# Performance work log

Measured on AMD Instinct MI355X. Metric: run time of the kernel, lower is better.

Reference implementation:

```python
import jax, jax.numpy as jnp
import numpy as np

E4M3_MAX = 448.0  # fp8_max_fwd for Format.HYBRID fprop tensors
MARGIN = 0        # DelayedScaling default


def _quantize_e4m3(t, s):
    # cast_to_fp8: scale, saturate-cast to E4M3; amax of the unscaled tensor
    q = (t * s).astype(jnp.float8_e4m3fn)
    amax = jnp.max(jnp.abs(t))
    return q, amax


def _sf_compute(amax, scale, fp8_max, margin):
    # faithful port of _default_sf_compute (including its tf.where ordering)
    exp = jnp.floor(jnp.log2(fp8_max / amax)) - margin
    sf = jnp.round(jnp.exp2(jnp.abs(exp)))
    sf = jnp.where(amax > 0.0, sf, scale)
    sf = jnp.where(jnp.isinf(amax), sf, scale)
    sf = jnp.where(exp < 0, 1.0 / sf, sf)
    return sf


def setup_inputs() -> dict:
    key = jax.random.key(0)
    k1, k2 = jax.random.split(key)
    M, K, N = 16384, 2048, 2048
    x = jax.random.normal(k1, (M, K), dtype=jnp.float32)
    kernel = jax.random.normal(k2, (K, N), dtype=jnp.float32) * 0.02
    scale = jnp.ones((2,), dtype=jnp.float32)
    scale_inv = jnp.ones((2,), dtype=jnp.float32)
    amax_history = jnp.zeros((1, 2), dtype=jnp.float32)
    return {"x": x, "kernel": kernel, "scale": scale,
            "scale_inv": scale_inv, "amax_history": amax_history}


def reference(x, kernel, scale, scale_inv, amax_history):
    # --- cast_to_fp8 for activation (index 0) and weight (index 1) ---
    x_q, amax_x = _quantize_e4m3(x, scale[0])          # [M, K] fp8
    w_q, amax_w = _quantize_e4m3(kernel.T, scale[1])   # [N, K] fp8 (B in row-major, gemm does B^T)
    new_scale_inv = jnp.stack([1.0 / scale[0], 1.0 / scale[1]])
    # record amaxes into most-recent slot of the history
    amax_history = amax_history.at[0, 0].set(amax_x).at[0, 1].set(amax_w)

    # --- fp8_matmul: D = (A * A_scale_inv) @ (B * B_scale_inv)^T ---
    out = jnp.matmul(x_q.astype(jnp.float32), w_q.astype(jnp.float32).T)
    out = out * (new_scale_inv[0] * new_scale_inv[1])  # [M, N]

    # --- fused_amax_and_scale_update (amax_compute_algo='most_recent') ---
    amax = amax_history[0]
    rolled = jnp.roll(amax_history, -1, axis=0).at[0].set(0.0)
    new_scale = _sf_compute(amax, scale, E4M3_MAX, MARGIN)
    return out, new_scale, rolled
```

## Files before the change

kernel.cpp:

```cpp
#include <hip/hip_runtime.h>
#include <cstdint>

#define M_DIM 16384
#define K_DIM 2048
#define N_DIM 2048

typedef float f32x4 __attribute__((ext_vector_type(4)));
typedef int   i32x8 __attribute__((ext_vector_type(8)));

__global__ __launch_bounds__(256) void quant_x_kernel(
    const float4* __restrict__ x, uint4* __restrict__ xq,
    const float* __restrict__ scale, unsigned int* __restrict__ amax)
{
    const int gid = blockIdx.x * 256 + threadIdx.x;
    const float s = scale[0];
    float m = 0.0f;
#pragma unroll
    for (int j = 0; j < 8; ++j) {
        float4 v = x[gid + j * 1048576];
        m = fmaxf(m, fmaxf(fmaxf(fabsf(v.x), fabsf(v.y)),
                           fmaxf(fabsf(v.z), fabsf(v.w))));
        unsigned int p0 = __builtin_amdgcn_cvt_pk_fp8_f32(v.x * s, v.y * s, 0, false);
        unsigned int p  = __builtin_amdgcn_cvt_pk_fp8_f32(v.z * s, v.w * s, p0, true);
        ((unsigned int*)xq)[gid + j * 1048576] = p;
    }

#pragma unroll
    for (int off = 32; off > 0; off >>= 1)
        m = fmaxf(m, __shfl_down(m, off, 64));
    __shared__ float red[4];
    if ((threadIdx.x & 63) == 0) red[threadIdx.x >> 6] = m;
    __syncthreads();
    if (threadIdx.x == 0) {
        m = fmaxf(fmaxf(red[0], red[1]), fmaxf(red[2], red[3]));
        atomicMax(amax, __float_as_uint(m));
    }
}

__global__ __launch_bounds__(256) void quant_w_kernel(
    const float* __restrict__ w, uint8_t* __restrict__ wq,
    const float* __restrict__ scale, unsigned int* __restrict__ amax)
{
    __shared__ float tile[64][68];
    const int t = threadIdx.x;
    const int nb = blockIdx.x * 64;
    const int kb = blockIdx.y * 64;
    const float s = scale[1];
    float m = 0.0f;
#pragma unroll
    for (int j = 0; j < 4; ++j) {
        int f = j * 256 + t;
        int row = f >> 4;
        int c4 = f & 15;
        float4 v = *(const float4*)(w + (size_t)(kb + row) * N_DIM + nb + c4 * 4);
        m = fmaxf(m, fmaxf(fmaxf(fabsf(v.x), fabsf(v.y)),
                           fmaxf(fabsf(v.z), fabsf(v.w))));
        *(float4*)(&tile[row][c4 * 4]) = v;
    }
    __syncthreads();
    const int n = t >> 2, c = t & 3;
    unsigned int pk[4];
#pragma unroll
    for (int jj = 0; jj < 4; ++jj) {
        float f0 = tile[c * 16 + jj * 4 + 0][n] * s;
        float f1 = tile[c * 16 + jj * 4 + 1][n] * s;
        float f2 = tile[c * 16 + jj * 4 + 2][n] * s;
        float f3 = tile[c * 16 + jj * 4 + 3][n] * s;
        unsigned int p = __builtin_amdgcn_cvt_pk_fp8_f32(f0, f1, 0, false);
        pk[jj] = __builtin_amdgcn_cvt_pk_fp8_f32(f2, f3, p, true);
    }
    *(uint4*)(wq + (size_t)(nb + n) * K_DIM + kb + c * 16) = make_uint4(pk[0], pk[1], pk[2], pk[3]);

#pragma unroll
    for (int off = 32; off > 0; off >>= 1)
        m = fmaxf(m, __shfl_down(m, off, 64));
    __shared__ float red[4];
    if ((t & 63) == 0) red[t >> 6] = m;
    __syncthreads();
    if (t == 0) {
        m = fmaxf(fmaxf(red[0], red[1]), fmaxf(red[2], red[3]));
        atomicMax(amax, __float_as_uint(m));
    }
}

__global__ __launch_bounds__(256) void gemm_fp8_kernel(
    const uint8_t* __restrict__ Aq, const uint8_t* __restrict__ Bq,
    const float* __restrict__ scale, float* __restrict__ C)
{
    __shared__ uint8_t lds[65536];
    const int tid  = threadIdx.x;
    const int wave = tid >> 6;
    const int lane = tid & 63;
    const int wm = wave >> 1, wn = wave & 1;
    const int q = lane >> 4, r = lane & 15;

    const int blk = blockIdx.x;
    const int xcd = blk & 7;
    const int idx = blk >> 3;
    const int bm  = xcd * 16 + (idx >> 4);
    const int bn  = idx & 15;

    const size_t a_base = (size_t)bm * 128 * K_DIM;
    const size_t b_base = (size_t)bn * 128 * K_DIM;

    int srow[4], skoff[4], sdst[4];
#pragma unroll
    for (int j = 0; j < 4; ++j) {
        const int s = j * 4 + wave;
        srow[j]  = (s >> 1) * 16 + (lane & 15);
        skoff[j] = (lane >> 4) * 32 + (s & 1) * 16;
        sdst[j]  = s * 1024 + lane * 16;
    }

    f32x4 acc[4][4];
#pragma unroll
    for (int i = 0; i < 4; ++i)
#pragma unroll
        for (int j = 0; j < 4; ++j) acc[i][j] = (f32x4){0.f, 0.f, 0.f, 0.f};

    const int SONE = 0x7F7F7F7F;

    auto issue = [&](int kt, int b) {
        const size_t kg = (size_t)kt * 128;
        uint8_t* base = lds + b * 32768;
#pragma unroll
        for (int j = 0; j < 4; ++j) {
            const uint8_t* ga = Aq + a_base + (size_t)srow[j] * K_DIM + kg + skoff[j];
            const uint8_t* gb = Bq + b_base + (size_t)srow[j] * K_DIM + kg + skoff[j];
            __builtin_amdgcn_global_load_lds(
                (const __attribute__((address_space(1))) uint32_t*)ga,
                (__attribute__((address_space(3))) uint32_t*)(base + sdst[j]), 16, 0, 0);
            __builtin_amdgcn_global_load_lds(
                (const __attribute__((address_space(1))) uint32_t*)gb,
                (__attribute__((address_space(3))) uint32_t*)(base + 16384 + sdst[j]), 16, 0, 0);
        }
    };

    issue(0, 0);

    for (int kt = 0; kt < K_DIM / 128; ++kt) {
        __syncthreads();
        if (kt + 1 < K_DIM / 128) issue(kt + 1, (kt + 1) & 1);

        const uint8_t* base = lds + (kt & 1) * 32768;
        i32x8 a_frag[4], b_frag[4];
#pragma unroll
        for (int mi = 0; mi < 4; ++mi) {
            const uint8_t* pa = base + (wm * 4 + mi) * 2048 + lane * 16;
            int4 lo = *(const int4*)pa;
            int4 hi = *(const int4*)(pa + 1024);
            a_frag[mi] = (i32x8){lo.x, lo.y, lo.z, lo.w, hi.x, hi.y, hi.z, hi.w};
        }
#pragma unroll
        for (int ni = 0; ni < 4; ++ni) {
            const uint8_t* pb = base + 16384 + (wn * 4 + ni) * 2048 + lane * 16;
            int4 lo = *(const int4*)pb;
            int4 hi = *(const int4*)(pb + 1024);
            b_frag[ni] = (i32x8){lo.x, lo.y, lo.z, lo.w, hi.x, hi.y, hi.z, hi.w};
        }
#pragma unroll
        for (int mi = 0; mi < 4; ++mi)
#pragma unroll
            for (int ni = 0; ni < 4; ++ni)
                acc[mi][ni] = __builtin_amdgcn_mfma_scale_f32_16x16x128_f8f6f4(
                    a_frag[mi], b_frag[ni], acc[mi][ni],
                    0 , 0 ,
                    0, SONE, 0, SONE);
    }

    const float sinv = (1.0f / scale[0]) * (1.0f / scale[1]);
#pragma unroll
    for (int mi = 0; mi < 4; ++mi) {
#pragma unroll
        for (int ni = 0; ni < 4; ++ni) {
            const int col  = bn * 128 + wn * 64 + ni * 16 + r;
            const int row0 = bm * 128 + wm * 64 + mi * 16 + q * 4;
#pragma unroll
            for (int rr = 0; rr < 4; ++rr)
                __builtin_nontemporal_store(acc[mi][ni][rr] * sinv,
                    &C[(size_t)(row0 + rr) * N_DIM + col]);
        }
    }
}

__global__ void finalize_kernel(const float* __restrict__ scale,
                                const unsigned int* __restrict__ amax_bits,
                                float* __restrict__ out_tail)
{
    const int i = threadIdx.x;
    if (i < 2) {
        const float amax = __uint_as_float(amax_bits[i]);
        const float sc = scale[i];
        const float e = floorf(log2f(448.0f / amax));
        float sf = roundf(exp2f(fabsf(e)));
        sf = (amax > 0.0f) ? sf : sc;
        sf = isinf(amax) ? sf : sc;
        if (e < 0.0f) sf = 1.0f / sf;
        out_tail[i] = sf;
        out_tail[2 + i] = 0.0f;
    }
}

extern "C" void kernel_launch(void* const* d_in, const int* in_sizes, int n_in,
                              void* d_out, int out_size, void* d_ws, size_t ws_size,
                              hipStream_t stream)
{
    const float* x     = (const float*)d_in[0];
    const float* w     = (const float*)d_in[1];
    const float* scale = (const float*)d_in[2];

    uint8_t* ws = (uint8_t*)d_ws;
    uint8_t* xq = ws;
    uint8_t* wq = ws + (size_t)M_DIM * K_DIM;
    unsigned int* amax = (unsigned int*)(ws + (size_t)M_DIM * K_DIM + (size_t)N_DIM * K_DIM);

    hipMemsetAsync(amax, 0, 2 * sizeof(unsigned int), stream);

    quant_x_kernel<<<4096, 256, 0, stream>>>(
        (const float4*)x, (uint4*)xq, scale, amax);

    dim3 gw(N_DIM / 64, K_DIM / 64);
    quant_w_kernel<<<gw, 256, 0, stream>>>(w, wq, scale, amax + 1);

    gemm_fp8_kernel<<<2048, 256, 0, stream>>>(xq, wq, scale, (float*)d_out);

    finalize_kernel<<<1, 64, 0, stream>>>(scale, amax,
                                          (float*)d_out + (size_t)M_DIM * N_DIM);
}
```

Baseline: 382.4 us.

## Load GEMM fragments directly from global memory, dropping LDS staging

The fp8 GEMM no longer stages A/B tiles through double-buffered LDS with global_load_lds and barriers. Each lane now loads its MFMA fragments straight from global memory, relying on L1/L2 for reuse across waves, and the k-loop is unrolled by two. The epilogue also switches from nontemporal stores to plain stores. This removes barrier and LDS traffic, but it loses explicit prefetch and cross-wave sharing, so global and L2 traffic may rise and load latency may be exposed.

After: 486.5 us. 1.27x slower.

```diff
diff --git a/kernel.cpp b/kernel.cpp
--- a/kernel.cpp
+++ b/kernel.cpp
@@ -87,7 +87,6 @@
     const uint8_t* __restrict__ Aq, const uint8_t* __restrict__ Bq,
     const float* __restrict__ scale, float* __restrict__ C)
 {
-    __shared__ uint8_t lds[65536];
     const int tid  = threadIdx.x;
     const int wave = tid >> 6;
     const int lane = tid & 63;
@@ -100,17 +99,8 @@
     const int bm  = xcd * 16 + (idx >> 4);
     const int bn  = idx & 15;
 
-    const size_t a_base = (size_t)bm * 128 * K_DIM;
-    const size_t b_base = (size_t)bn * 128 * K_DIM;
-
-    int srow[4], skoff[4], sdst[4];
-#pragma unroll
-    for (int j = 0; j < 4; ++j) {
-        const int s = j * 4 + wave;
-        srow[j]  = (s >> 1) * 16 + (lane & 15);
-        skoff[j] = (lane >> 4) * 32 + (s & 1) * 16;
-        sdst[j]  = s * 1024 + lane * 16;
-    }
+    const uint8_t* pa = Aq + (size_t)(bm * 128 + wm * 64 + r) * K_DIM + q * 32;
+    const uint8_t* pb = Bq + (size_t)(bn * 128 + wn * 64 + r) * K_DIM + q * 32;
 
     f32x4 acc[4][4];
 #pragma unroll
@@ -120,42 +110,22 @@
 
     const int SONE = 0x7F7F7F7F;
 
-    auto issue = [&](int kt, int b) {
-        const size_t kg = (size_t)kt * 128;
-        uint8_t* base = lds + b * 32768;
-#pragma unroll
-        for (int j = 0; j < 4; ++j) {
-            const uint8_t* ga = Aq + a_base + (size_t)srow[j] * K_DIM + kg + skoff[j];
-            const uint8_t* gb = Bq + b_base + (size_t)srow[j] * K_DIM + kg + skoff[j];
-            __builtin_amdgcn_global_load_lds(
-                (const __attribute__((address_space(1))) uint32_t*)ga,
-                (__attribute__((address_space(3))) uint32_t*)(base + sdst[j]), 16, 0, 0);
-            __builtin_amdgcn_global_load_lds(
-                (const __attribute__((address_space(1))) uint32_t*)gb,
-                (__attribute__((address_space(3))) uint32_t*)(base + 16384 + sdst[j]), 16, 0, 0);
-        }
-    };
-
-    issue(0, 0);
-
+#pragma unroll 2
     for (int kt = 0; kt < K_DIM / 128; ++kt) {
-        __syncthreads();
-        if (kt + 1 < K_DIM / 128) issue(kt + 1, (kt + 1) & 1);
-
-        const uint8_t* base = lds + (kt & 1) * 32768;
+        const int ko = kt * 128;
         i32x8 a_frag[4], b_frag[4];
 #pragma unroll
         for (int mi = 0; mi < 4; ++mi) {
-            const uint8_t* pa = base + (wm * 4 + mi) * 2048 + lane * 16;
-            int4 lo = *(const int4*)pa;
-            int4 hi = *(const int4*)(pa + 1024);
+            const uint8_t* p = pa + (size_t)mi * 16 * K_DIM + ko;
+            int4 lo = *(const int4*)p;
+            int4 hi = *(const int4*)(p + 16);
             a_frag[mi] = (i32x8){lo.x, lo.y, lo.z, lo.w, hi.x, hi.y, hi.z, hi.w};
         }
 #pragma unroll
         for (int ni = 0; ni < 4; ++ni) {
-            const uint8_t* pb = base + 16384 + (wn * 4 + ni) * 2048 + lane * 16;
-            int4 lo = *(const int4*)pb;
-            int4 hi = *(const int4*)(pb + 1024);
+            const uint8_t* p = pb + (size_t)ni * 16 * K_DIM + ko;
+            int4 lo = *(const int4*)p;
+            int4 hi = *(const int4*)(p + 16);
             b_frag[ni] = (i32x8){lo.x, lo.y, lo.z, lo.w, hi.x, hi.y, hi.z, hi.w};
         }
 #pragma unroll
@@ -177,8 +147,7 @@
             const int row0 = bm * 128 + wm * 64 + mi * 16 + q * 4;
 #pragma unroll
             for (int rr = 0; rr < 4; ++rr)
-                __builtin_nontemporal_store(acc[mi][ni][rr] * sinv,
-                    &C[(size_t)(row0 + rr) * N_DIM + col]);
+                C[(size_t)(row0 + rr) * N_DIM + col] = acc[mi][ni][rr] * sinv;
         }
     }
 }
```
